# Performance work log

Hardware: AMD Instinct MI355X
Metric: run time of the kernel (lower is better)

## Reference

```python
import jax, jax.numpy as jnp
import numpy as np

V, B, L, NG = 50000, 128, 350, 3        # vocab, batch(docs), doc length, n-gram window
D, H, C = 768, 256, 20                  # bert dim, num_hidden, class_num
HEADS, LAYERS, K, ALPHA = 8, 2, 3, 0.15 # GAT heads/layers, diffusion hops k, alpha


def setup_inputs() -> dict:
    rng = np.random.default_rng(0)
    # per-doc graphs: 350 unique word-ids per doc (nodes), n-gram window edges
    node_ids = np.stack([rng.choice(V, L, replace=False) for _ in range(B)]).ravel()
    src_b, dst_b = [], []
    for i in range(L):
        for j in range(max(0, i - NG), min(L, i + NG + 1)):
            src_b.append(i); dst_b.append(j)
    src_b, dst_b = np.asarray(src_b), np.asarray(dst_b)
    off = (np.arange(B) * L)[:, None]
    edge_src = (src_b[None, :] + off).ravel()
    edge_dst = (dst_b[None, :] + off).ravel()
    graph_id = np.repeat(np.arange(B), L)

    ks = jax.random.split(jax.random.key(0), 8)
    f32 = jnp.float32
    return {
        'node_ids': jnp.asarray(node_ids, jnp.int32),
        'edge_src': jnp.asarray(edge_src, jnp.int32),
        'edge_dst': jnp.asarray(edge_dst, jnp.int32),
        'graph_id': jnp.asarray(graph_id, jnp.int32),
        'emb':    (jax.random.normal(ks[0], (V, D), f32) * 0.02),
        'W1':     (jax.random.normal(ks[1], (D, H), f32) / np.sqrt(D)).astype(f32),
        'b1':     jnp.zeros((H,), f32),
        'W2':     (jax.random.normal(ks[2], (H, C), f32) / np.sqrt(H)).astype(f32),
        'b2':     jnp.zeros((C,), f32),
        'gat_W':  (jax.random.normal(ks[3], (LAYERS, HEADS, C, C), f32) / np.sqrt(C)).astype(f32),
        'a_src':  (jax.random.normal(ks[4], (LAYERS, HEADS, C), f32) * 0.1),
        'a_dst':  (jax.random.normal(ks[5], (LAYERS, HEADS, C), f32) * 0.1),
        'w_gate': (jax.random.normal(ks[6], (C,), f32) / np.sqrt(C)).astype(f32),
        'b_gate': jnp.zeros((), f32),
    }


def _gat_layer(h, W, a_s, a_d, src, dst, N):
    # h: [N,C]; W: [Hd,C,C]; a_s/a_d: [Hd,C]
    z = jnp.einsum('nc,hcd->hnd', h, W)                     # [Hd,N,C]
    e = jax.nn.leaky_relu(jnp.einsum('hnd,hd->hn', z, a_s)[:, src]
                          + jnp.einsum('hnd,hd->hn', z, a_d)[:, dst], 0.2)  # [Hd,E]

    def segsoftmax(ev):  # edge softmax over incoming edges at each dst node
        m = jax.ops.segment_max(ev, dst, num_segments=N)
        ex = jnp.exp(ev - m[dst])
        s = jax.ops.segment_sum(ex, dst, num_segments=N)
        return ex / (s[dst] + 1e-9)

    att = jax.vmap(segsoftmax)(e)                           # [Hd,E]

    def diffuse(zh, ah):  # attention diffusion: Z_t = (1-a) A Z_{t-1} + a Z_0
        zt = zh
        for _ in range(K):
            agg = jax.ops.segment_sum(ah[:, None] * zt[src], dst, num_segments=N)
            zt = (1.0 - ALPHA) * agg + ALPHA * zh
        return zt

    out = jax.vmap(diffuse)(z, att)                         # [Hd,N,C]
    return jax.nn.elu(out).mean(axis=0)                     # merge='mean'


def reference(node_ids, edge_src, edge_dst, graph_id, emb, W1, b1, W2, b2,
              gat_W, a_src, a_dst, w_gate, b_gate):
    N = node_ids.shape[0]
    x = emb[node_ids]                                       # [N,768] gather
    x = jax.nn.relu(x @ W1 + b1)                            # linear1 + ReLU
    h = x @ W2 + b2                                         # linear2 -> [N,C]
    for l in range(LAYERS):
        h = _gat_layer(h, gat_W[l], a_src[l], a_dst[l], edge_src, edge_dst, N)
    gate = jax.nn.sigmoid(h @ w_gate + b_gate)[:, None]     # WeightAndSum gate
    return jax.ops.segment_sum(gate * h, graph_id, num_segments=B)  # [B,C]
```

## Files before the change

### kernel.cpp

```cpp
#include <hip/hip_runtime.h>
#include <hip/hip_bf16.h>
#include <cstddef>

#define NB_NODES 44800
#define NDOCS 128
#define DLEN 350
#define DIM 768
#define HID 256
#define NCLS 20
#define NHEADS 8
#define ZROW 352

typedef __bf16 v8bf __attribute__((ext_vector_type(8)));
typedef __bf16 v4bf __attribute__((ext_vector_type(4)));
typedef __bf16 v2bf __attribute__((ext_vector_type(2)));
typedef float v4f __attribute__((ext_vector_type(4)));
typedef float v2f __attribute__((ext_vector_type(2)));

__global__ __launch_bounds__(256) void k_transpose(const float* __restrict__ W1,
                                                   __bf16* __restrict__ W1T) {
  int idx = blockIdx.x * 256 + threadIdx.x;
  int n = idx / 768, k = idx - n * 768;
  W1T[idx] = (__bf16)W1[k * 256 + n];
}

__global__ __launch_bounds__(256) void k_mlp(
    const int* __restrict__ node_ids, const float* __restrict__ emb,
    const __bf16* __restrict__ W1T, const float* __restrict__ b1,
    const float* __restrict__ W2, const float* __restrict__ b2,
    float* __restrict__ h0) {
  __shared__ __align__(16) char smem[26880];
  float*  xs = (float*)smem;
  __bf16* w2s = (__bf16*)(smem + 16640);
  int tid = threadIdx.x;
  int wave = tid >> 6, lane = tid & 63;
  int quad = lane >> 4, l16 = lane & 15;
  int m0 = blockIdx.x * 32;

  for (int i = tid; i < HID * NCLS; i += 256) w2s[i] = (__bf16)W2[i];

  const float* rp0 = emb + (size_t)node_ids[m0 + l16] * DIM + quad * 8;
  const float* rp1 = emb + (size_t)node_ids[m0 + 16 + l16] * DIM + quad * 8;

  v4f acc[2][4];
#pragma unroll
  for (int ms = 0; ms < 2; ++ms)
#pragma unroll
    for (int j = 0; j < 4; ++j) acc[ms][j] = (v4f){0.f, 0.f, 0.f, 0.f};

#pragma unroll 3
  for (int kc = 0; kc < 12; ++kc) {
    int kb = kc * 64;
#pragma unroll
    for (int ks = 0; ks < 2; ++ks) {
      int ko = kb + ks * 32;
      v4f a0l = *(const v4f*)(rp0 + ko);
      v4f a0h = *(const v4f*)(rp0 + ko + 4);
      v4f a1l = *(const v4f*)(rp1 + ko);
      v4f a1h = *(const v4f*)(rp1 + ko + 4);
      v8bf bv[4];
#pragma unroll
      for (int j = 0; j < 4; ++j)
        bv[j] = *(const v8bf*)(W1T + (size_t)(wave * 64 + j * 16 + l16) * DIM + ko + quad * 8);
      v8bf af0, af1;
#pragma unroll
      for (int e = 0; e < 4; ++e) {
        af0[e] = (__bf16)a0l[e]; af0[4 + e] = (__bf16)a0h[e];
        af1[e] = (__bf16)a1l[e]; af1[4 + e] = (__bf16)a1h[e];
      }
#pragma unroll
      for (int j = 0; j < 4; ++j)
        acc[0][j] = __builtin_amdgcn_mfma_f32_16x16x32_bf16(af0, bv[j], acc[0][j], 0, 0, 0);
#pragma unroll
      for (int j = 0; j < 4; ++j)
        acc[1][j] = __builtin_amdgcn_mfma_f32_16x16x32_bf16(af1, bv[j], acc[1][j], 0, 0, 0);
    }
  }

#pragma unroll
  for (int ms = 0; ms < 2; ++ms) {
    if (ms) __syncthreads();
#pragma unroll
    for (int j = 0; j < 4; ++j) {
      int col = wave * 64 + j * 16 + l16;
      float bb = b1[col];
#pragma unroll
      for (int r = 0; r < 4; ++r) {
        int lr = quad * 4 + r;
        float v = acc[ms][j][r] + bb;
        xs[lr * 260 + col] = v > 0.f ? v : 0.f;
      }
    }
    __syncthreads();
    if (tid < 160) {
      int m = tid / 10, c0 = (tid % 10) * 2;
      float s0 = b2[c0], s1 = b2[c0 + 1];
      for (int k = 0; k < HID; ++k) {
        float x = xs[m * 260 + k];
        v2bf w = *(const v2bf*)(w2s + k * NCLS + c0);
        s0 += x * (float)w[0]; s1 += x * (float)w[1];
      }
      v2f o; o[0] = s0; o[1] = s1;
      *(v2f*)(h0 + (size_t)(m0 + ms * 16 + m) * NCLS + c0) = o;
    }
  }
}

__global__ __launch_bounds__(384) void k_gat(
    const float* __restrict__ hin, const float* __restrict__ gatW,
    const float* __restrict__ a_src, const float* __restrict__ a_dst,
    int layer, float* __restrict__ zout) {
  __shared__ float zT[NCLS * ZROW];
  __shared__ float asv[DLEN], adv[DLEN];
  int tid = threadIdx.x;
  int head = blockIdx.x & 7;
  int doc = blockIdx.x >> 3;
  const float* W  = gatW  + (size_t)(layer * NHEADS + head) * NCLS * NCLS;
  const float* av = a_src + (layer * NHEADS + head) * NCLS;
  const float* dv = a_dst + (layer * NHEADS + head) * NCLS;
  int r = tid;
  bool act = r < DLEN;

  float z0[NCLS];
  if (act) {
    const float* hr = hin + ((size_t)doc * DLEN + r) * NCLS;
    float h[NCLS];
#pragma unroll
    for (int q = 0; q < 5; ++q) {
      v4f t = *(const v4f*)(hr + q * 4);
#pragma unroll
      for (int e = 0; e < 4; ++e) h[q * 4 + e] = t[e];
    }
    float zacc[NCLS];
#pragma unroll
    for (int d = 0; d < NCLS; ++d) zacc[d] = 0.f;
#pragma unroll
    for (int c = 0; c < NCLS; ++c) {
      float hc = h[c];
#pragma unroll
      for (int d = 0; d < NCLS; ++d) zacc[d] += hc * W[c * NCLS + d];
    }
    float sa = 0.f, sd = 0.f;
#pragma unroll
    for (int d = 0; d < NCLS; ++d) { sa += zacc[d] * av[d]; sd += zacc[d] * dv[d]; }
    asv[r] = sa; adv[r] = sd;
#pragma unroll
    for (int c = 0; c < NCLS; ++c) zT[c * ZROW + r] = zacc[c];
#pragma unroll
    for (int d = 0; d < NCLS; ++d) z0[d] = zacc[d];
  }
  __syncthreads();

  float att[7];
  if (act) {
    float ad = adv[r];
    float e[7]; float m = -1e30f;
#pragma unroll
    for (int j = 0; j < 7; ++j) {
      int s = r - 3 + j;
      bool valid = (s >= 0) && (s < DLEN);
      float x = valid ? asv[s] + ad : -1e30f;
      x = x > 0.f ? x : 0.2f * x;
      e[j] = valid ? x : -1e30f;
      if (e[j] > m) m = e[j];
    }
    float sum = 0.f;
#pragma unroll
    for (int j = 0; j < 7; ++j) {
      float ex = (e[j] > -1e29f) ? expf(e[j] - m) : 0.f;
      e[j] = ex; sum += ex;
    }
    float inv = 1.f / (sum + 1e-9f);
#pragma unroll
    for (int j = 0; j < 7; ++j) att[j] = e[j] * inv;
  }

  float vn[NCLS];
  for (int hop = 0; hop < 3; ++hop) {
    if (act) {
      float agg[NCLS];
#pragma unroll
      for (int c = 0; c < NCLS; ++c) agg[c] = 0.f;
#pragma unroll
      for (int j = 0; j < 7; ++j) {
        int s = r - 3 + j;
        s = s < 0 ? 0 : (s > DLEN - 1 ? DLEN - 1 : s);
        float a = att[j];
#pragma unroll
        for (int c = 0; c < NCLS; ++c) agg[c] += a * zT[c * ZROW + s];
      }
#pragma unroll
      for (int c = 0; c < NCLS; ++c) vn[c] = 0.85f * agg[c] + 0.15f * z0[c];
    }
    if (hop < 2) {
      __syncthreads();
      if (act) {
#pragma unroll
        for (int c = 0; c < NCLS; ++c) zT[c * ZROW + r] = vn[c];
      }
      __syncthreads();
    }
  }

  if (act) {
    float* og = zout + ((size_t)head * NB_NODES + (size_t)doc * DLEN + r) * NCLS;
#pragma unroll
    for (int q = 0; q < 5; ++q) {
      v4f t;
#pragma unroll
      for (int e = 0; e < 4; ++e) {
        float x = vn[q * 4 + e];
        t[e] = x > 0.f ? x : expf(x) - 1.f;
      }
      *(v4f*)(og + q * 4) = t;
    }
  }
}

__global__ __launch_bounds__(256) void k_headmean(
    const float* __restrict__ eluzt, float* __restrict__ hout) {
  int idx = blockIdx.x * 256 + threadIdx.x;
  v4f s = (v4f){0.f, 0.f, 0.f, 0.f};
#pragma unroll
  for (int h = 0; h < NHEADS; ++h)
    s += ((const v4f*)eluzt)[(size_t)h * (NB_NODES * NCLS / 4) + idx];
  v4f o; o[0] = s[0] * 0.125f; o[1] = s[1] * 0.125f; o[2] = s[2] * 0.125f; o[3] = s[3] * 0.125f;
  ((v4f*)hout)[idx] = o;
}

__global__ __launch_bounds__(384) void k_hm_pool(
    const float* __restrict__ eluzt, const float* __restrict__ w_gate,
    const float* __restrict__ b_gate, float* __restrict__ out) {
  __shared__ float red[6][NCLS];
  int tid = threadIdx.x;
  int doc = blockIdx.x;
  int r = tid;
  bool act = r < DLEN;

  float wg[NCLS];
#pragma unroll
  for (int c = 0; c < NCLS; ++c) wg[c] = w_gate[c];
  float contrib[NCLS];
#pragma unroll
  for (int c = 0; c < NCLS; ++c) contrib[c] = 0.f;
  if (act) {
    float hm[NCLS];
#pragma unroll
    for (int c = 0; c < NCLS; ++c) hm[c] = 0.f;
#pragma unroll
    for (int hd = 0; hd < NHEADS; ++hd) {
      const float* p = eluzt + ((size_t)hd * NB_NODES + (size_t)doc * DLEN + r) * NCLS;
#pragma unroll
      for (int q = 0; q < 5; ++q) {
        v4f t = *(const v4f*)(p + q * 4);
#pragma unroll
        for (int e = 0; e < 4; ++e) hm[q * 4 + e] += t[e];
      }
    }
    float d = b_gate[0];
#pragma unroll
    for (int c = 0; c < NCLS; ++c) { hm[c] *= 0.125f; d += hm[c] * wg[c]; }
    float g = 1.f / (1.f + expf(-d));
#pragma unroll
    for (int c = 0; c < NCLS; ++c) contrib[c] = g * hm[c];
  }
#pragma unroll
  for (int off = 32; off > 0; off >>= 1)
#pragma unroll
    for (int c = 0; c < NCLS; ++c) contrib[c] += __shfl_down(contrib[c], off);
  int wave = tid >> 6, lane = tid & 63;
  if (lane == 0)
#pragma unroll
    for (int c = 0; c < NCLS; ++c) red[wave][c] = contrib[c];
  __syncthreads();
  if (tid < NCLS) {
    float s = 0.f;
#pragma unroll
    for (int w = 0; w < 6; ++w) s += red[w][tid];
    out[doc * NCLS + tid] = s;
  }
}

extern "C" void kernel_launch(void* const* d_in, const int* in_sizes, int n_in,
                              void* d_out, int out_size, void* d_ws, size_t ws_size,
                              hipStream_t stream) {
  const int* node_ids = (const int*)d_in[0];
  const float* emb    = (const float*)d_in[4];
  const float* W1     = (const float*)d_in[5];
  const float* b1     = (const float*)d_in[6];
  const float* W2     = (const float*)d_in[7];
  const float* b2     = (const float*)d_in[8];
  const float* gatW   = (const float*)d_in[9];
  const float* a_src  = (const float*)d_in[10];
  const float* a_dst  = (const float*)d_in[11];
  const float* w_gate = (const float*)d_in[12];
  const float* b_gate = (const float*)d_in[13];
  float* out = (float*)d_out;
  char* ws = (char*)d_ws;

  __bf16* W1T = (__bf16*)(ws + 0);
  float* hA  = (float*)(ws + 393216);
  float* hB  = (float*)(ws + 3977216);
  float* zt  = (float*)(ws + 7561216);

  k_transpose<<<768, 256, 0, stream>>>(W1, W1T);
  k_mlp<<<NB_NODES / 32, 256, 0, stream>>>(node_ids, emb, W1T, b1, W2, b2, hA);
  k_gat<<<NDOCS * NHEADS, 384, 0, stream>>>(hA, gatW, a_src, a_dst, 0, zt);
  k_headmean<<<(NB_NODES * NCLS / 4) / 256, 256, 0, stream>>>(zt, hB);
  k_gat<<<NDOCS * NHEADS, 384, 0, stream>>>(hB, gatW, a_src, a_dst, 1, zt);
  k_hm_pool<<<NDOCS, 384, 0, stream>>>(zt, w_gate, b_gate, out);
}
```

Baseline: 421.9 us.

## Stage gathered embeddings in LDS and pre-pack W1 into MFMA fragment order

The MLP kernel now gathers each block's 32 embedding rows cooperatively with coalesced 16-byte loads, converts them to bf16 and stores them in padded shared memory. The MFMA loop then reads A fragments from LDS. W1 is pre-packed so that each lane's B fragment is one contiguous load per k-step, replacing strided row reads of the transposed weights. The aim is to cut uncoalesced global traffic in the gather-GEMM. The cost is 51 KB of LDS per block, which may limit occupancy, plus an extra barrier.

Result: faster. 351.0 us (-16.8%).

```diff
diff --git a/kernel.cpp b/kernel.cpp
--- a/kernel.cpp
+++ b/kernel.cpp
@@ -10,6 +10,7 @@
 #define NCLS 20
 #define NHEADS 8
 #define ZROW 352
+#define ASTR 800
 
 typedef __bf16 v8bf __attribute__((ext_vector_type(8)));
 typedef __bf16 v4bf __attribute__((ext_vector_type(4)));
@@ -17,65 +18,80 @@
 typedef float v4f __attribute__((ext_vector_type(4)));
 typedef float v2f __attribute__((ext_vector_type(2)));
 
-__global__ __launch_bounds__(256) void k_transpose(const float* __restrict__ W1,
-                                                   __bf16* __restrict__ W1T) {
+__global__ __launch_bounds__(256) void k_pack(const float* __restrict__ W1,
+                                              __bf16* __restrict__ W1P) {
   int idx = blockIdx.x * 256 + threadIdx.x;
-  int n = idx / 768, k = idx - n * 768;
-  W1T[idx] = (__bf16)W1[k * 256 + n];
+  int e = idx & 7;
+  int l = (idx >> 3) & 63;
+  int rest = idx >> 9;
+  int ks = rest % 24;
+  int cb = rest / 24;
+  int k = ks * 32 + (l >> 4) * 8 + e;
+  int col = cb * 16 + (l & 15);
+  W1P[idx] = (__bf16)W1[k * 256 + col];
 }
 
 __global__ __launch_bounds__(256) void k_mlp(
     const int* __restrict__ node_ids, const float* __restrict__ emb,
-    const __bf16* __restrict__ W1T, const float* __restrict__ b1,
+    const __bf16* __restrict__ W1P, const float* __restrict__ b1,
     const float* __restrict__ W2, const float* __restrict__ b2,
     float* __restrict__ h0) {
-  __shared__ __align__(16) char smem[26880];
-  float*  xs = (float*)smem;
+  __shared__ __align__(16) char smem[51200];
+  __bf16* Asl = (__bf16*)smem;
+  float*  xs  = (float*)smem;
   __bf16* w2s = (__bf16*)(smem + 16640);
   int tid = threadIdx.x;
   int wave = tid >> 6, lane = tid & 63;
   int quad = lane >> 4, l16 = lane & 15;
   int m0 = blockIdx.x * 32;
 
+  {
+    int r0 = wave * 8;
+    int nid[8];
+#pragma unroll
+    for (int rr = 0; rr < 8; ++rr) nid[rr] = node_ids[m0 + r0 + rr];
+#pragma unroll
+    for (int p = 0; p < 3; ++p) {
+      v4f t[8];
+#pragma unroll
+      for (int rr = 0; rr < 8; ++rr)
+        t[rr] = *(const v4f*)(emb + (size_t)nid[rr] * DIM + p * 256 + lane * 4);
+#pragma unroll
+      for (int rr = 0; rr < 8; ++rr) {
+        v4bf b;
+#pragma unroll
+        for (int e = 0; e < 4; ++e) b[e] = (__bf16)t[rr][e];
+        *(v4bf*)(Asl + (r0 + rr) * ASTR + p * 256 + lane * 4) = b;
+      }
+    }
+  }
+
+  v4f acc[2][4];
+#pragma unroll
+  for (int ms = 0; ms < 2; ++ms)
+#pragma unroll
+    for (int j = 0; j < 4; ++j) acc[ms][j] = (v4f){0.f, 0.f, 0.f, 0.f};
+
+  __syncthreads();
+
+  const __bf16* wpB = W1P + (size_t)wave * 49152 + lane * 8;
+#pragma unroll 4
+  for (int ks = 0; ks < 24; ++ks) {
+    v8bf a0 = *(const v8bf*)(Asl + l16 * ASTR + ks * 32 + quad * 8);
+    v8bf a1 = *(const v8bf*)(Asl + (16 + l16) * ASTR + ks * 32 + quad * 8);
+    v8bf bv[4];
+#pragma unroll
+    for (int j = 0; j < 4; ++j)
+      bv[j] = *(const v8bf*)(wpB + j * 12288 + ks * 512);
+#pragma unroll
+    for (int j = 0; j < 4; ++j) {
+      acc[0][j] = __builtin_amdgcn_mfma_f32_16x16x32_bf16(a0, bv[j], acc[0][j], 0, 0, 0);
+      acc[1][j] = __builtin_amdgcn_mfma_f32_16x16x32_bf16(a1, bv[j], acc[1][j], 0, 0, 0);
+    }
+  }
+
+  __syncthreads();
   for (int i = tid; i < HID * NCLS; i += 256) w2s[i] = (__bf16)W2[i];
-
-  const float* rp0 = emb + (size_t)node_ids[m0 + l16] * DIM + quad * 8;
-  const float* rp1 = emb + (size_t)node_ids[m0 + 16 + l16] * DIM + quad * 8;
-
-  v4f acc[2][4];
-#pragma unroll
-  for (int ms = 0; ms < 2; ++ms)
-#pragma unroll
-    for (int j = 0; j < 4; ++j) acc[ms][j] = (v4f){0.f, 0.f, 0.f, 0.f};
-
-#pragma unroll 3
-  for (int kc = 0; kc < 12; ++kc) {
-    int kb = kc * 64;
-#pragma unroll
-    for (int ks = 0; ks < 2; ++ks) {
-      int ko = kb + ks * 32;
-      v4f a0l = *(const v4f*)(rp0 + ko);
-      v4f a0h = *(const v4f*)(rp0 + ko + 4);
-      v4f a1l = *(const v4f*)(rp1 + ko);
-      v4f a1h = *(const v4f*)(rp1 + ko + 4);
-      v8bf bv[4];
-#pragma unroll
-      for (int j = 0; j < 4; ++j)
-        bv[j] = *(const v8bf*)(W1T + (size_t)(wave * 64 + j * 16 + l16) * DIM + ko + quad * 8);
-      v8bf af0, af1;
-#pragma unroll
-      for (int e = 0; e < 4; ++e) {
-        af0[e] = (__bf16)a0l[e]; af0[4 + e] = (__bf16)a0h[e];
-        af1[e] = (__bf16)a1l[e]; af1[4 + e] = (__bf16)a1h[e];
-      }
-#pragma unroll
-      for (int j = 0; j < 4; ++j)
-        acc[0][j] = __builtin_amdgcn_mfma_f32_16x16x32_bf16(af0, bv[j], acc[0][j], 0, 0, 0);
-#pragma unroll
-      for (int j = 0; j < 4; ++j)
-        acc[1][j] = __builtin_amdgcn_mfma_f32_16x16x32_bf16(af1, bv[j], acc[1][j], 0, 0, 0);
-    }
-  }
 
 #pragma unroll
   for (int ms = 0; ms < 2; ++ms) {
@@ -298,13 +314,13 @@
   float* out = (float*)d_out;
   char* ws = (char*)d_ws;
 
-  __bf16* W1T = (__bf16*)(ws + 0);
+  __bf16* W1P = (__bf16*)(ws + 0);
   float* hA  = (float*)(ws + 393216);
   float* hB  = (float*)(ws + 3977216);
   float* zt  = (float*)(ws + 7561216);
 
-  k_transpose<<<768, 256, 0, stream>>>(W1, W1T);
-  k_mlp<<<NB_NODES / 32, 256, 0, stream>>>(node_ids, emb, W1T, b1, W2, b2, hA);
+  k_pack<<<768, 256, 0, stream>>>(W1, W1P);
+  k_mlp<<<NB_NODES / 32, 256, 0, stream>>>(node_ids, emb, W1P, b1, W2, b2, hA);
   k_gat<<<NDOCS * NHEADS, 384, 0, stream>>>(hA, gatW, a_src, a_dst, 0, zt);
   k_headmean<<<(NB_NODES * NCLS / 4) / 256, 256, 0, stream>>>(zt, hB);
   k_gat<<<NDOCS * NHEADS, 384, 0, stream>>>(hB, gatW, a_src, a_dst, 1, zt);
```
